# Performance work log

Measured on AMD Instinct MI355X. Metric: run time of the kernel, lower is better.

Reference implementation:

```python
import jax, jax.numpy as jnp
import numpy as np

N_NODES = 50000
N_EDGES = 800000
NODE_DIM = 32
EDGE_DIM = 16
HIDDEN = 64


def setup_inputs() -> dict:
    key = jax.random.key(0)
    ks = jax.random.split(key, 7)
    h = jax.random.normal(ks[0], (N_NODES, HIDDEN), dtype=jnp.float32)
    nf = jax.random.normal(ks[1], (N_NODES, NODE_DIM), dtype=jnp.float32)
    ef = jax.random.normal(ks[2], (N_EDGES, EDGE_DIM), dtype=jnp.float32)
    src = jax.random.randint(ks[3], (N_EDGES,), 0, N_NODES, dtype=jnp.int32)
    dst = jax.random.randint(ks[4], (N_EDGES,), 0, N_NODES, dtype=jnp.int32)
    # torch Linear weights: [out_features, in_features]
    in1 = HIDDEN + 2 * NODE_DIM + EDGE_DIM  # 144
    W1 = jax.random.normal(ks[5], (HIDDEN, in1), dtype=jnp.float32) * (1.0 / np.sqrt(in1))
    W2 = jax.random.normal(ks[6], (HIDDEN, HIDDEN), dtype=jnp.float32) * (1.0 / np.sqrt(HIDDEN))
    return {"h": h, "nf": nf, "ef": ef, "src": src, "dst": dst, "W1": W1, "W2": W2}


def reference(h, nf, ef, src, dst, W1, W2):
    n = nf.shape[0]
    # per-edge message: concat(dst.x, edge.x, src.h)  -> [E, node+edge+hidden]
    m_e = jnp.concatenate([nf[dst], ef, h[src]], axis=-1)
    # mailbox sum per destination node
    m = jax.ops.segment_sum(m_e, dst, num_segments=n)  # [N, node+edge+hidden]
    z = jnp.concatenate([nf, m], axis=-1)              # [N, hidden+2*node+edge]
    new_h = jax.nn.relu(z @ W1.T) @ W2.T               # [N, hidden]
    # DGL update_all only updates nodes that received at least one message
    deg = jax.ops.segment_sum(jnp.ones_like(dst, dtype=jnp.float32), dst, num_segments=n)
    return jnp.where(deg[:, None] > 0, new_h, h)
```

## Files before the change

### kernel.cpp

```cpp
#include <hip/hip_runtime.h>

#define NDIM 32
#define EDIM 16
#define NHID 64
#define NIN1 144
#define SCHUNK 1024
#define SPT 4

__device__ __forceinline__ unsigned pk2(float a, float b) {
  unsigned ua = __float_as_uint(a);
  unsigned ub = __float_as_uint(b);
  ua = (ua + 0x7FFFu + ((ua >> 16) & 1u)) >> 16;
  ub = (ub + 0x7FFFu + ((ub >> 16) & 1u)) >> 16;
  return ua | (ub << 16);
}
__device__ __forceinline__ float lo16(unsigned u) { return __uint_as_float(u << 16); }
__device__ __forceinline__ float hi16(unsigned u) { return __uint_as_float(u & 0xFFFF0000u); }

#define ACC8(A, V)                                   \
  do {                                               \
    A[0] += lo16((V).x); A[1] += hi16((V).x);        \
    A[2] += lo16((V).y); A[3] += hi16((V).y);        \
    A[4] += lo16((V).z); A[5] += hi16((V).z);        \
    A[6] += lo16((V).w); A[7] += hi16((V).w);        \
  } while (0)

__global__ __launch_bounds__(256) void sse_hist(
    const int* __restrict__ dst, int* __restrict__ counts,
    int* __restrict__ rank,
    const float* __restrict__ W1, float* __restrict__ W1T,
    const float* __restrict__ W2, float* __restrict__ W2T, int E) {
  int t = blockIdx.x * 256 + threadIdx.x;
  if (t < NHID * NIN1) {
    int r = t / NIN1, k = t - r * NIN1;
    W1T[k * NHID + r] = W1[t];
  } else if (t < NHID * NIN1 + NHID * NHID) {
    int i = t - NHID * NIN1;
    int r = i >> 6, k = i & 63;
    W2T[k * NHID + r] = W2[i];
  }
  int ebase = blockIdx.x * 1024 + threadIdx.x;
  int r[4];
#pragma unroll
  for (int i = 0; i < 4; ++i) {
    int e = ebase + i * 256;
    if (e < E) r[i] = atomicAdd(&counts[dst[e]], 1);
  }
#pragma unroll
  for (int i = 0; i < 4; ++i) {
    int e = ebase + i * 256;
    if (e < E) rank[e] = r[i];
  }
}

__global__ __launch_bounds__(256) void sse_scan_part(
    const int* __restrict__ counts, int* __restrict__ bsum, int N) {
  __shared__ int ws[4];
  int t = threadIdx.x;
  int base = blockIdx.x * SCHUNK + t * SPT;
  int s = 0;
#pragma unroll
  for (int i = 0; i < SPT; ++i) {
    int idx = base + i;
    if (idx < N) s += counts[idx];
  }
  int v = s;
#pragma unroll
  for (int off = 1; off < 64; off <<= 1) v += __shfl_xor(v, off, 64);
  if ((t & 63) == 0) ws[t >> 6] = v;
  __syncthreads();
  if (t == 0) bsum[blockIdx.x] = ws[0] + ws[1] + ws[2] + ws[3];
}

__global__ __launch_bounds__(256) void sse_scan_final(
    const int* __restrict__ counts, const int* __restrict__ bsum,
    int* __restrict__ starts, int N, int nb) {
  __shared__ int ws[4];
  int t = threadIdx.x;
  int lane = t & 63, w = t >> 6;
  int boff = 0;
  for (int j = 0; j < (int)blockIdx.x; ++j) boff += bsum[j];
  int base = blockIdx.x * SCHUNK + t * SPT;
  int c[SPT];
  int s = 0;
#pragma unroll
  for (int i = 0; i < SPT; ++i) {
    int idx = base + i;
    c[i] = (idx < N) ? counts[idx] : 0;
    s += c[i];
  }
  int incl = s;
#pragma unroll
  for (int off = 1; off < 64; off <<= 1) {
    int u = __shfl_up(incl, off, 64);
    if (lane >= off) incl += u;
  }
  if (lane == 63) ws[w] = incl;
  __syncthreads();
  int woff = 0;
#pragma unroll
  for (int j = 0; j < 4; ++j)
    if (j < w) woff += ws[j];
  int run = boff + woff + (incl - s);
#pragma unroll
  for (int i = 0; i < SPT; ++i) {
    int idx = base + i;
    if (idx < N) {
      starts[idx] = run;
      run += c[i];
    }
  }
  if ((int)blockIdx.x == nb - 1 && t == 0)
    starts[N] = boff + ws[0] + ws[1] + ws[2] + ws[3];
}

__global__ __launch_bounds__(256) void sse_build(
    const int* __restrict__ src, const int* __restrict__ dst,
    const int* __restrict__ rank, const int* __restrict__ starts,
    const float* __restrict__ ef, int* __restrict__ ssrc,
    uint4* __restrict__ sef16,
    const float* __restrict__ h, uint4* __restrict__ h16,
    int E, int N) {
  int ebase = blockIdx.x * 1024 + threadIdx.x;
  const float4* ef4 = (const float4*)ef;
#pragma unroll
  for (int i = 0; i < 4; ++i) {
    int e = ebase + i * 256;
    if (e < E) {
      int d = dst[e];
      int pos = starts[d] + rank[e];
      ssrc[pos] = src[e];
      float4 x = ef4[(size_t)e * 4 + 0];
      float4 y = ef4[(size_t)e * 4 + 1];
      float4 zq = ef4[(size_t)e * 4 + 2];
      float4 wq = ef4[(size_t)e * 4 + 3];
      uint4 o0, o1;
      o0.x = pk2(x.x, x.y);  o0.y = pk2(x.z, x.w);
      o0.z = pk2(y.x, y.y);  o0.w = pk2(y.z, y.w);
      o1.x = pk2(zq.x, zq.y); o1.y = pk2(zq.z, zq.w);
      o1.z = pk2(wq.x, wq.y); o1.w = pk2(wq.z, wq.w);
      sef16[(size_t)pos * 2 + 0] = o0;
      sef16[(size_t)pos * 2 + 1] = o1;
    }
  }
  int t = blockIdx.x * 256 + threadIdx.x;
  int T = gridDim.x * 256;
  const float4* hf4 = (const float4*)h;
  int NH = N * 8;
  for (int i = t; i < NH; i += T) {
    float4 x = hf4[2 * i], y = hf4[2 * i + 1];
    uint4 o;
    o.x = pk2(x.x, x.y); o.y = pk2(x.z, x.w);
    o.z = pk2(y.x, y.y); o.w = pk2(y.z, y.w);
    h16[i] = o;
  }
}

__global__ __launch_bounds__(256) void sse_gather(
    const uint4* __restrict__ h16, const int* __restrict__ ssrc,
    const uint4* __restrict__ sef16,
    const int* __restrict__ starts,
    uint4* __restrict__ efsum16, uint4* __restrict__ hsum16, int N) {
  int w = threadIdx.x >> 6;
  int lane = threadIdx.x & 63;
  int node = blockIdx.x * 4 + w;
  if (node >= N) return;
  int st = starts[node], en = starts[node + 1];

  int q8 = lane >> 3, m = lane & 7;
  int eh = lane >> 1;
  float acc[8], ea8[8];
#pragma unroll
  for (int i = 0; i < 8; ++i) { acc[i] = 0.f; ea8[i] = 0.f; }

  for (int base = st; base < en; base += 64) {
    int C = en - base; C = C > 64 ? 64 : C;
    int myS = (lane < C) ? ssrc[base + lane] : 0;
    int nr = (C + 31) >> 5;
    for (int r = 0; r < nr; ++r) {
      int b = r * 32;
      int i0 = b + q8, i1 = b + 8 + q8, i2 = b + 16 + q8, i3 = b + 24 + q8;
      int s0 = __shfl(myS, i0, 64);
      int s1 = __shfl(myS, i1, 64);
      int s2 = __shfl(myS, i2, 64);
      int s3 = __shfl(myS, i3, 64);
      int ie = b + eh;
      uint4 v0 = h16[(size_t)s0 * 8 + m];
      uint4 v1 = h16[(size_t)s1 * 8 + m];
      uint4 v2 = h16[(size_t)s2 * 8 + m];
      uint4 v3 = h16[(size_t)s3 * 8 + m];
      if (ie < C) {
        uint4 ev = sef16[((size_t)(base + b)) * 2 + lane];
        ACC8(ea8, ev);
      }
      if (i0 < C) ACC8(acc, v0);
      if (i1 < C) ACC8(acc, v1);
      if (i2 < C) ACC8(acc, v2);
      if (i3 < C) ACC8(acc, v3);
    }
  }

#pragma unroll
  for (int off = 8; off < 64; off <<= 1)
#pragma unroll
    for (int i = 0; i < 8; ++i) acc[i] += __shfl_xor(acc[i], off, 64);
  if (lane < 8) {
    uint4 o;
    o.x = pk2(acc[0], acc[1]); o.y = pk2(acc[2], acc[3]);
    o.z = pk2(acc[4], acc[5]); o.w = pk2(acc[6], acc[7]);
    hsum16[(size_t)node * 8 + lane] = o;
  }
#pragma unroll
  for (int off = 2; off < 64; off <<= 1)
#pragma unroll
    for (int i = 0; i < 8; ++i) ea8[i] += __shfl_xor(ea8[i], off, 64);
  if (lane < 2) {
    uint4 o;
    o.x = pk2(ea8[0], ea8[1]); o.y = pk2(ea8[2], ea8[3]);
    o.z = pk2(ea8[4], ea8[5]); o.w = pk2(ea8[6], ea8[7]);
    efsum16[(size_t)node * 2 + lane] = o;
  }
}

__global__ __launch_bounds__(256) void sse_node(
    const float* __restrict__ h, const float* __restrict__ nf,
    const uint4* __restrict__ efsum16, const uint4* __restrict__ hsum16,
    const int* __restrict__ starts, const float* __restrict__ W1T,
    const float* __restrict__ W2T, float* __restrict__ out, int N) {
  __shared__ float4 zs[36 * 64];
  __shared__ float4 as[16 * 64];

  int tid = threadIdx.x;
  int lane = tid & 63;
  int w = __builtin_amdgcn_readfirstlane(tid) >> 6;

  int node = blockIdx.x * 64 + lane;
  int nodeC = node < N ? node : N - 1;

  if (w == 0) {
    int st = starts[nodeC], en = starts[nodeC + 1];
    float dg = (float)(en - st);
    const float4* nfr = (const float4*)(nf + (size_t)nodeC * NDIM);
#pragma unroll
    for (int k4 = 0; k4 < 8; ++k4) {
      float4 v = nfr[k4];
      zs[k4 * 64 + lane] = v;
      zs[(8 + k4) * 64 + lane] =
          make_float4(dg * v.x, dg * v.y, dg * v.z, dg * v.w);
    }
  } else if (w == 1) {
    uint4 a = efsum16[(size_t)nodeC * 2 + 0];
    uint4 b = efsum16[(size_t)nodeC * 2 + 1];
    zs[16 * 64 + lane] = make_float4(lo16(a.x), hi16(a.x), lo16(a.y), hi16(a.y));
    zs[17 * 64 + lane] = make_float4(lo16(a.z), hi16(a.z), lo16(a.w), hi16(a.w));
    zs[18 * 64 + lane] = make_float4(lo16(b.x), hi16(b.x), lo16(b.y), hi16(b.y));
    zs[19 * 64 + lane] = make_float4(lo16(b.z), hi16(b.z), lo16(b.w), hi16(b.w));
  } else if (w == 2) {
#pragma unroll
    for (int c = 0; c < 4; ++c) {
      uint4 u = hsum16[(size_t)nodeC * 8 + c];
      zs[(20 + 2 * c) * 64 + lane] =
          make_float4(lo16(u.x), hi16(u.x), lo16(u.y), hi16(u.y));
      zs[(21 + 2 * c) * 64 + lane] =
          make_float4(lo16(u.z), hi16(u.z), lo16(u.w), hi16(u.w));
    }
  } else {
#pragma unroll
    for (int c = 4; c < 8; ++c) {
      uint4 u = hsum16[(size_t)nodeC * 8 + c];
      zs[(20 + 2 * c) * 64 + lane] =
          make_float4(lo16(u.x), hi16(u.x), lo16(u.y), hi16(u.y));
      zs[(21 + 2 * c) * 64 + lane] =
          make_float4(lo16(u.z), hi16(u.z), lo16(u.w), hi16(u.w));
    }
  }
  __syncthreads();

  const float4* w1b = (const float4*)W1T + w * 4;
  float a[16];
#pragma unroll
  for (int j = 0; j < 16; ++j) a[j] = 0.f;

#pragma unroll 2
  for (int k4 = 0; k4 < 36; ++k4) {
    float4 zv = zs[k4 * 64 + lane];
#pragma unroll
    for (int kk = 0; kk < 4; ++kk) {
      int k = k4 * 4 + kk;
      float4 w0 = w1b[k * 16 + 0];
      float4 w1 = w1b[k * 16 + 1];
      float4 w2 = w1b[k * 16 + 2];
      float4 w3 = w1b[k * 16 + 3];
      float zk = kk == 0 ? zv.x : kk == 1 ? zv.y : kk == 2 ? zv.z : zv.w;
      a[0]  = fmaf(w0.x, zk, a[0]);
      a[1]  = fmaf(w0.y, zk, a[1]);
      a[2]  = fmaf(w0.z, zk, a[2]);
      a[3]  = fmaf(w0.w, zk, a[3]);
      a[4]  = fmaf(w1.x, zk, a[4]);
      a[5]  = fmaf(w1.y, zk, a[5]);
      a[6]  = fmaf(w1.z, zk, a[6]);
      a[7]  = fmaf(w1.w, zk, a[7]);
      a[8]  = fmaf(w2.x, zk, a[8]);
      a[9]  = fmaf(w2.y, zk, a[9]);
      a[10] = fmaf(w2.z, zk, a[10]);
      a[11] = fmaf(w2.w, zk, a[11]);
      a[12] = fmaf(w3.x, zk, a[12]);
      a[13] = fmaf(w3.y, zk, a[13]);
      a[14] = fmaf(w3.z, zk, a[14]);
      a[15] = fmaf(w3.w, zk, a[15]);
    }
  }

#pragma unroll
  for (int j4 = 0; j4 < 4; ++j4)
    as[(w * 4 + j4) * 64 + lane] =
        make_float4(fmaxf(a[j4 * 4 + 0], 0.f), fmaxf(a[j4 * 4 + 1], 0.f),
                    fmaxf(a[j4 * 4 + 2], 0.f), fmaxf(a[j4 * 4 + 3], 0.f));
  __syncthreads();

  const float4* w2b = (const float4*)W2T + w * 4;
  float o[16];
#pragma unroll
  for (int j = 0; j < 16; ++j) o[j] = 0.f;

#pragma unroll 2
  for (int kq = 0; kq < 16; ++kq) {
    float4 av = as[kq * 64 + lane];
#pragma unroll
    for (int kk = 0; kk < 4; ++kk) {
      int k = kq * 4 + kk;
      float4 w0 = w2b[k * 16 + 0];
      float4 w1 = w2b[k * 16 + 1];
      float4 w2 = w2b[k * 16 + 2];
      float4 w3 = w2b[k * 16 + 3];
      float ak = kk == 0 ? av.x : kk == 1 ? av.y : kk == 2 ? av.z : av.w;
      o[0]  = fmaf(w0.x, ak, o[0]);
      o[1]  = fmaf(w0.y, ak, o[1]);
      o[2]  = fmaf(w0.z, ak, o[2]);
      o[3]  = fmaf(w0.w, ak, o[3]);
      o[4]  = fmaf(w1.x, ak, o[4]);
      o[5]  = fmaf(w1.y, ak, o[5]);
      o[6]  = fmaf(w1.z, ak, o[6]);
      o[7]  = fmaf(w1.w, ak, o[7]);
      o[8]  = fmaf(w2.x, ak, o[8]);
      o[9]  = fmaf(w2.y, ak, o[9]);
      o[10] = fmaf(w2.z, ak, o[10]);
      o[11] = fmaf(w2.w, ak, o[11]);
      o[12] = fmaf(w3.x, ak, o[12]);
      o[13] = fmaf(w3.y, ak, o[13]);
      o[14] = fmaf(w3.z, ak, o[14]);
      o[15] = fmaf(w3.w, ak, o[15]);
    }
  }

  if (node < N) {
    int st = starts[node], en = starts[node + 1];
    float4* o4 = (float4*)(out + (size_t)node * NHID + w * 16);
    if (en - st == 0) {
      const float4* hr = (const float4*)(h + (size_t)node * NHID + w * 16);
#pragma unroll
      for (int j4 = 0; j4 < 4; ++j4) o4[j4] = hr[j4];
    } else {
#pragma unroll
      for (int j4 = 0; j4 < 4; ++j4)
        o4[j4] = make_float4(o[j4 * 4 + 0], o[j4 * 4 + 1], o[j4 * 4 + 2],
                             o[j4 * 4 + 3]);
    }
  }
}

extern "C" void kernel_launch(void* const* d_in, const int* in_sizes, int n_in,
                              void* d_out, int out_size, void* d_ws, size_t ws_size,
                              hipStream_t stream) {
  const float* h  = (const float*)d_in[0];
  const float* nf = (const float*)d_in[1];
  const float* ef = (const float*)d_in[2];
  const int*   src = (const int*)d_in[3];
  const int*   dst = (const int*)d_in[4];
  const float* W1 = (const float*)d_in[5];
  const float* W2 = (const float*)d_in[6];
  float* out = (float*)d_out;

  int N = in_sizes[0] / NHID;
  int E = in_sizes[3];

  char* p = (char*)d_ws;
  int* ssrc = (int*)p;                    p += (size_t)E * 4;
  uint4* sef16 = (uint4*)p;               p += (size_t)E * 32;
  int* counts = (int*)p;                  p += (size_t)N * 4;
  int* starts = (int*)p;                  p += (size_t)(N + 1) * 4;
  int* bsum = (int*)p;                    p += 64 * 4;
  float* W1T = (float*)p;                 p += (size_t)NIN1 * NHID * 4;
  float* W2T = (float*)p;                 p += (size_t)NHID * NHID * 4;
  p = (char*)(((size_t)p + 15) & ~(size_t)15);
  uint4* h16 = (uint4*)p;                 p += (size_t)N * 128;
  uint4* efsum16 = (uint4*)p;             p += (size_t)N * 32;
  uint4* hsum16 = (uint4*)p;              p += (size_t)N * 128;
  int* rank = (int*)hsum16;

  hipMemsetAsync(counts, 0, (size_t)N * sizeof(int), stream);

  int eblocks4 = (E + 1023) / 1024;
  int nb = (N + SCHUNK - 1) / SCHUNK;

  sse_hist<<<eblocks4, 256, 0, stream>>>(dst, counts, rank, W1, W1T, W2, W2T, E);
  sse_scan_part<<<nb, 256, 0, stream>>>(counts, bsum, N);
  sse_scan_final<<<nb, 256, 0, stream>>>(counts, bsum, starts, N, nb);
  sse_build<<<eblocks4, 256, 0, stream>>>(src, dst, rank, starts, ef, ssrc,
                                          sef16, h, h16, E, N);

  int gblocks = (N + 3) / 4;
  sse_gather<<<gblocks, 256, 0, stream>>>(h16, ssrc, sef16, starts,
                                          efsum16, hsum16, N);

  int nblocks = (N + 63) / 64;
  sse_node<<<nblocks, 256, 0, stream>>>(h, nf, efsum16, hsum16, starts, W1T,
                                        W2T, out, N);
}
```

Before: 265.6 us.

## Gather edge features by edge id instead of materialising sorted bf16 copy

```diff
diff --git a/kernel.cpp b/kernel.cpp
--- a/kernel.cpp
+++ b/kernel.cpp
@@ -25,12 +25,12 @@
     A[6] += lo16((V).w); A[7] += hi16((V).w);        \
   } while (0)
 
-__global__ __launch_bounds__(256) void sse_hist(
-    const int* __restrict__ dst, int* __restrict__ counts,
-    int* __restrict__ rank,
+__global__ __launch_bounds__(256) void sse_conv(
+    const float* __restrict__ h, uint4* __restrict__ h16,
     const float* __restrict__ W1, float* __restrict__ W1T,
-    const float* __restrict__ W2, float* __restrict__ W2T, int E) {
+    const float* __restrict__ W2, float* __restrict__ W2T, int N) {
   int t = blockIdx.x * 256 + threadIdx.x;
+  int T = gridDim.x * 256;
   if (t < NHID * NIN1) {
     int r = t / NIN1, k = t - r * NIN1;
     W1T[k * NHID + r] = W1[t];
@@ -39,6 +39,20 @@
     int r = i >> 6, k = i & 63;
     W2T[k * NHID + r] = W2[i];
   }
+  const float4* hf4 = (const float4*)h;
+  int NH = N * 8;
+  for (int i = t; i < NH; i += T) {
+    float4 x = hf4[2 * i], y = hf4[2 * i + 1];
+    uint4 o;
+    o.x = pk2(x.x, x.y); o.y = pk2(x.z, x.w);
+    o.z = pk2(y.x, y.y); o.w = pk2(y.z, y.w);
+    h16[i] = o;
+  }
+}
+
+__global__ __launch_bounds__(256) void sse_hist(
+    const int* __restrict__ dst, int* __restrict__ counts,
+    int* __restrict__ rank, int E) {
   int ebase = blockIdx.x * 1024 + threadIdx.x;
   int r[4];
 #pragma unroll
@@ -117,49 +131,22 @@
 __global__ __launch_bounds__(256) void sse_build(
     const int* __restrict__ src, const int* __restrict__ dst,
     const int* __restrict__ rank, const int* __restrict__ starts,
-    const float* __restrict__ ef, int* __restrict__ ssrc,
-    uint4* __restrict__ sef16,
-    const float* __restrict__ h, uint4* __restrict__ h16,
-    int E, int N) {
+    int2* __restrict__ sedge, int E) {
   int ebase = blockIdx.x * 1024 + threadIdx.x;
-  const float4* ef4 = (const float4*)ef;
 #pragma unroll
   for (int i = 0; i < 4; ++i) {
     int e = ebase + i * 256;
     if (e < E) {
       int d = dst[e];
       int pos = starts[d] + rank[e];
-      ssrc[pos] = src[e];
-      float4 x = ef4[(size_t)e * 4 + 0];
-      float4 y = ef4[(size_t)e * 4 + 1];
-      float4 zq = ef4[(size_t)e * 4 + 2];
-      float4 wq = ef4[(size_t)e * 4 + 3];
-      uint4 o0, o1;
-      o0.x = pk2(x.x, x.y);  o0.y = pk2(x.z, x.w);
-      o0.z = pk2(y.x, y.y);  o0.w = pk2(y.z, y.w);
-      o1.x = pk2(zq.x, zq.y); o1.y = pk2(zq.z, zq.w);
-      o1.z = pk2(wq.x, wq.y); o1.w = pk2(wq.z, wq.w);
-      sef16[(size_t)pos * 2 + 0] = o0;
-      sef16[(size_t)pos * 2 + 1] = o1;
-    }
-  }
-  int t = blockIdx.x * 256 + threadIdx.x;
-  int T = gridDim.x * 256;
-  const float4* hf4 = (const float4*)h;
-  int NH = N * 8;
-  for (int i = t; i < NH; i += T) {
-    float4 x = hf4[2 * i], y = hf4[2 * i + 1];
-    uint4 o;
-    o.x = pk2(x.x, x.y); o.y = pk2(x.z, x.w);
-    o.z = pk2(y.x, y.y); o.w = pk2(y.z, y.w);
-    h16[i] = o;
+      sedge[pos] = make_int2(src[e], e);
+    }
   }
 }
 
 __global__ __launch_bounds__(256) void sse_gather(
-    const uint4* __restrict__ h16, const int* __restrict__ ssrc,
-    const uint4* __restrict__ sef16,
-    const int* __restrict__ starts,
+    const uint4* __restrict__ h16, const float* __restrict__ ef,
+    const int2* __restrict__ sedge, const int* __restrict__ starts,
     uint4* __restrict__ efsum16, uint4* __restrict__ hsum16, int N) {
   int w = threadIdx.x >> 6;
   int lane = threadIdx.x & 63;
@@ -167,15 +154,19 @@
   if (node >= N) return;
   int st = starts[node], en = starts[node + 1];
 
+  const float4* ef4 = (const float4*)ef;
   int q8 = lane >> 3, m = lane & 7;
-  int eh = lane >> 1;
-  float acc[8], ea8[8];
-#pragma unroll
-  for (int i = 0; i < 8; ++i) { acc[i] = 0.f; ea8[i] = 0.f; }
+  int eq = lane >> 2, em = lane & 3;
+
+  float acc[8];
+#pragma unroll
+  for (int i = 0; i < 8; ++i) acc[i] = 0.f;
+  float4 ea = make_float4(0.f, 0.f, 0.f, 0.f);
 
   for (int base = st; base < en; base += 64) {
     int C = en - base; C = C > 64 ? 64 : C;
-    int myS = (lane < C) ? ssrc[base + lane] : 0;
+    int2 seg = (lane < C) ? sedge[base + lane] : make_int2(0, 0);
+    int myS = seg.x, myE = seg.y;
     int nr = (C + 31) >> 5;
     for (int r = 0; r < nr; ++r) {
       int b = r * 32;
@@ -184,19 +175,21 @@
       int s1 = __shfl(myS, i1, 64);
       int s2 = __shfl(myS, i2, 64);
       int s3 = __shfl(myS, i3, 64);
-      int ie = b + eh;
+      int e0 = b + eq, e1 = b + 16 + eq;
+      int id0 = __shfl(myE, e0, 64);
+      int id1 = __shfl(myE, e1, 64);
       uint4 v0 = h16[(size_t)s0 * 8 + m];
       uint4 v1 = h16[(size_t)s1 * 8 + m];
       uint4 v2 = h16[(size_t)s2 * 8 + m];
       uint4 v3 = h16[(size_t)s3 * 8 + m];
-      if (ie < C) {
-        uint4 ev = sef16[((size_t)(base + b)) * 2 + lane];
-        ACC8(ea8, ev);
-      }
+      float4 x0 = ef4[(size_t)id0 * 4 + em];
+      float4 x1 = ef4[(size_t)id1 * 4 + em];
       if (i0 < C) ACC8(acc, v0);
       if (i1 < C) ACC8(acc, v1);
       if (i2 < C) ACC8(acc, v2);
       if (i3 < C) ACC8(acc, v3);
+      if (e0 < C) { ea.x += x0.x; ea.y += x0.y; ea.z += x0.z; ea.w += x0.w; }
+      if (e1 < C) { ea.x += x1.x; ea.y += x1.y; ea.z += x1.z; ea.w += x1.w; }
     }
   }
 
@@ -211,14 +204,21 @@
     hsum16[(size_t)node * 8 + lane] = o;
   }
 #pragma unroll
-  for (int off = 2; off < 64; off <<= 1)
-#pragma unroll
-    for (int i = 0; i < 8; ++i) ea8[i] += __shfl_xor(ea8[i], off, 64);
-  if (lane < 2) {
+  for (int off = 4; off < 64; off <<= 1) {
+    ea.x += __shfl_xor(ea.x, off, 64);
+    ea.y += __shfl_xor(ea.y, off, 64);
+    ea.z += __shfl_xor(ea.z, off, 64);
+    ea.w += __shfl_xor(ea.w, off, 64);
+  }
+  float bx = __shfl_xor(ea.x, 1, 64);
+  float by = __shfl_xor(ea.y, 1, 64);
+  float bz = __shfl_xor(ea.z, 1, 64);
+  float bw = __shfl_xor(ea.w, 1, 64);
+  if (lane < 4 && (lane & 1) == 0) {
     uint4 o;
-    o.x = pk2(ea8[0], ea8[1]); o.y = pk2(ea8[2], ea8[3]);
-    o.z = pk2(ea8[4], ea8[5]); o.w = pk2(ea8[6], ea8[7]);
-    efsum16[(size_t)node * 2 + lane] = o;
+    o.x = pk2(ea.x, ea.y); o.y = pk2(ea.z, ea.w);
+    o.z = pk2(bx, by);     o.w = pk2(bz, bw);
+    efsum16[(size_t)node * 2 + (lane >> 1)] = o;
   }
 }
 
@@ -385,8 +385,7 @@
   int E = in_sizes[3];
 
   char* p = (char*)d_ws;
-  int* ssrc = (int*)p;                    p += (size_t)E * 4;
-  uint4* sef16 = (uint4*)p;               p += (size_t)E * 32;
+  int2* sedge = (int2*)p;                 p += (size_t)E * 8;
   int* counts = (int*)p;                  p += (size_t)N * 4;
   int* starts = (int*)p;                  p += (size_t)(N + 1) * 4;
   int* bsum = (int*)p;                    p += 64 * 4;
@@ -403,14 +402,14 @@
   int eblocks4 = (E + 1023) / 1024;
   int nb = (N + SCHUNK - 1) / SCHUNK;
 
-  sse_hist<<<eblocks4, 256, 0, stream>>>(dst, counts, rank, W1, W1T, W2, W2T, E);
+  sse_conv<<<1024, 256, 0, stream>>>(h, h16, W1, W1T, W2, W2T, N);
+  sse_hist<<<eblocks4, 256, 0, stream>>>(dst, counts, rank, E);
   sse_scan_part<<<nb, 256, 0, stream>>>(counts, bsum, N);
   sse_scan_final<<<nb, 256, 0, stream>>>(counts, bsum, starts, N, nb);
-  sse_build<<<eblocks4, 256, 0, stream>>>(src, dst, rank, starts, ef, ssrc,
-                                          sef16, h, h16, E, N);
+  sse_build<<<eblocks4, 256, 0, stream>>>(src, dst, rank, starts, sedge, E);
 
   int gblocks = (N + 3) / 4;
-  sse_gather<<<gblocks, 256, 0, stream>>>(h16, ssrc, sef16, starts,
+  sse_gather<<<gblocks, 256, 0, stream>>>(h16, ef, sedge, starts,
                                           efsum16, hsum16, N);
 
   int nblocks = (N + 63) / 64;
```

After: 232.3 us. 12.5% less time.
